# Kernel tuning notes

Hardware: AMD Instinct MI355X
Metric: run time of the kernel (lower is better)

Reference implementation:

```python
import jax, jax.numpy as jnp
import numpy as np

N_HEADS = 16
SEG_LEN = 512
MSG_LEN = 1536
T_TOTAL = SEG_LEN + MSG_LEN  # 2048


def _build_mask(T):
    # rows < SEG_LEN: attend to all cols < SEG_LEN (full, non-causal block)
    # rows >= SEG_LEN: standard causal (cols <= row)
    rows = jnp.arange(T)[:, None]
    cols = jnp.arange(T)[None, :]
    mask = jnp.where(rows < SEG_LEN, cols < SEG_LEN, cols <= rows)
    return mask  # [T, T] bool


def setup_inputs() -> dict:
    key = jax.random.key(0)
    k1, k2, k3 = jax.random.split(key, 3)
    B, T, E = 4, T_TOTAL, 1024
    x = jax.random.normal(k1, (B, T, E), dtype=jnp.float32)
    W_qkv = jax.random.normal(k2, (E, 3 * E), dtype=jnp.float32) * (1.0 / np.sqrt(E))
    b_qkv = jnp.zeros((3 * E,), dtype=jnp.float32)
    W_proj = jax.random.normal(k3, (E, E), dtype=jnp.float32) * (1.0 / np.sqrt(E))
    b_proj = jnp.zeros((E,), dtype=jnp.float32)
    return {"x": x, "W_qkv": W_qkv, "b_qkv": b_qkv, "W_proj": W_proj, "b_proj": b_proj}


def reference(x, W_qkv, b_qkv, W_proj, b_proj):
    B, T, E = x.shape
    H = N_HEADS
    D = E // H
    qkv = x @ W_qkv + b_qkv  # [B, T, 3E]
    q, k, v = jnp.split(qkv, 3, axis=-1)
    # [B, H, T, D]
    q = q.reshape(B, T, H, D).transpose(0, 2, 1, 3)
    k = k.reshape(B, T, H, D).transpose(0, 2, 1, 3)
    v = v.reshape(B, T, H, D).transpose(0, 2, 1, 3)
    att = jnp.einsum("bhqd,bhkd->bhqk", q, k) * (1.0 / np.sqrt(D))
    mask = _build_mask(T)  # [T, T]
    att = jnp.where(mask[None, None], att, jnp.float32(-jnp.inf))
    att = jax.nn.softmax(att, axis=-1)
    y = jnp.einsum("bhqk,bhkd->bhqd", att, v)
    y = y.transpose(0, 2, 1, 3).reshape(B, T, E)
    return y @ W_proj + b_proj
```

## Files before the change

### kernel.cpp

```cpp
#include <hip/hip_runtime.h>


typedef _Float16 f16;
typedef _Float16 f16x4 __attribute__((ext_vector_type(4)));
typedef _Float16 f16x8 __attribute__((ext_vector_type(8)));
typedef float f32x4 __attribute__((ext_vector_type(4)));

#define MFMA16x32(a, b, c) __builtin_amdgcn_mfma_f32_16x16x32_f16(a, b, c, 0, 0, 0)
#define MFMA16x16(a, b, c) __builtin_amdgcn_mfma_f32_16x16x16f16(a, b, c, 0, 0, 0)

__device__ __forceinline__ void gload_lds16(const void* g, void* l) {
  __builtin_amdgcn_global_load_lds(
      (__attribute__((address_space(1))) void*)g,
      (__attribute__((address_space(3))) void*)l, 16, 0, 0);
}


__global__ __launch_bounds__(256) void k_prep(
    const float* __restrict__ x, f16* __restrict__ xh,
    const float* __restrict__ Wq, f16* __restrict__ Wqt,
    const float* __restrict__ Wp, f16* __restrict__ Wpt) {
  __shared__ float tile[32][33];
  const int bid = blockIdx.x;
  if (bid < 8192) {
    int i = bid * 256 + threadIdx.x;
    float4 v = ((const float4*)x)[i];
    f16x4 o = {(f16)v.x, (f16)v.y, (f16)v.z, (f16)v.w};
    ((f16x4*)xh)[i] = o;
    return;
  }
  const float* W;
  f16* Wt;
  int Ndim, bx, by;
  if (bid < 8192 + 3072) {
    int r = bid - 8192;
    W = Wq; Wt = Wqt; Ndim = 3072; bx = r % 96; by = r / 96;
  } else {
    int r = bid - 11264;
    W = Wp; Wt = Wpt; Ndim = 1024; bx = r % 32; by = r / 32;
  }
  const int tx = threadIdx.x & 31, ty = threadIdx.x >> 5;
  const int n = bx * 32 + tx;
  const int k0 = by * 32;
  for (int j = ty; j < 32; j += 8)
    tile[j][tx] = W[(size_t)(k0 + j) * Ndim + n];
  __syncthreads();
  const int k = k0 + tx;
  for (int j = ty; j < 32; j += 8)
    Wt[(size_t)(bx * 32 + j) * 1024 + k] = (f16)tile[tx][j];
}


__global__ __launch_bounds__(512) void k_gemm_qkv(
    const f16* __restrict__ A, const f16* __restrict__ Bt,
    const float* __restrict__ bias,
    f16* __restrict__ Qo, f16* __restrict__ Ko, f16* __restrict__ Vo) {
  constexpr int KD = 1024;
  __shared__ __align__(16) f16 smem[(128 + 256) * 64];
  f16* As = smem;
  f16* Bs = smem + 128 * 64;
  const int tid = threadIdx.x;
  const int wave = tid >> 6, lane = tid & 63;
  const int g = lane >> 4, l16 = lane & 15;
  const int m0 = blockIdx.y * 128, n0 = blockIdx.x * 256;
  const int wm = (wave >> 2) * 64, wn = (wave & 3) * 64;
  const int srow = wave * 8 + (lane >> 3);
  const int skc = ((lane & 7) ^ (lane >> 3)) * 8;

  f32x4 acc[4][4] = {};

  for (int k0 = 0; k0 < KD; k0 += 64) {
    __syncthreads();
    for (int it = 0; it < 2; ++it)
      gload_lds16(A + (size_t)(m0 + it * 64 + srow) * KD + k0 + skc,
                  As + (it * 64 + wave * 8) * 64);
    for (int it = 0; it < 4; ++it)
      gload_lds16(Bt + (size_t)(n0 + it * 64 + srow) * KD + k0 + skc,
                  Bs + (it * 64 + wave * 8) * 64);
    __syncthreads();
    for (int kk = 0; kk < 64; kk += 32) {
      const int ks = kk >> 3;
      f16x8 af[4], bf[4];
      for (int mi = 0; mi < 4; ++mi) {
        int R = wm + mi * 16 + l16, sw = R & 7;
        af[mi] = *(const f16x8*)(As + R * 64 + ((ks + g) ^ sw) * 8);
      }
      for (int ni = 0; ni < 4; ++ni) {
        int R = wn + ni * 16 + l16, sw = R & 7;
        bf[ni] = *(const f16x8*)(Bs + R * 64 + ((ks + g) ^ sw) * 8);
      }
      for (int mi = 0; mi < 4; ++mi)
        for (int ni = 0; ni < 4; ++ni)
          acc[mi][ni] = MFMA16x32(af[mi], bf[ni], acc[mi][ni]);
    }
  }

  const int nsub = n0 + wn;
  const int part = nsub >> 10;
  const int h    = (nsub >> 6) & 15;
  const int mg   = m0 + wm;
  const int b    = mg >> 11;
  const int tb   = mg & 2047;
  const size_t bh = (size_t)(b * 16 + h);

  float bv[4];
  for (int ni = 0; ni < 4; ++ni) bv[ni] = bias[nsub + ni * 16 + l16];

  __syncthreads();
  f16* Es = smem + (wave & 3) * 4096;
  const int rrow = lane >> 3, rj = lane & 7;

  for (int phase = 0; phase < 2; ++phase) {
    if ((wave >> 2) == phase) {
      for (int mi = 0; mi < 4; ++mi)
        for (int ni = 0; ni < 4; ++ni)
          for (int r = 0; r < 4; ++r) {
            f16 hv = (f16)(acc[mi][ni][r] + bv[ni]);
            int mrow = mi * 16 + g * 4 + r, ncol = ni * 16 + l16;
            if (part == 2)
              Es[ncol * 64 + (mrow ^ ((ncol & 7) << 3))] = hv;
            else
              Es[mrow * 64 + (ncol ^ ((mrow & 7) << 3))] = hv;
          }
      for (int p = 0; p < 8; ++p) {
        int row = p * 8 + rrow;
        f16x8 vv = *(const f16x8*)(Es + row * 64 + (rj ^ (row & 7)) * 8);
        int rcol = rj * 8;
        if (part == 0)
          *(f16x8*)(Qo + (bh * 2048 + tb + row) * 64 + rcol) = vv;
        else if (part == 1)
          *(f16x8*)(Ko + (bh * 2048 + tb + row) * 64 + rcol) = vv;
        else
          *(f16x8*)(Vo + (bh * 64 + row) * 2048 + tb + rcol) = vv;
      }
    }
    __syncthreads();
  }
}


__global__ __launch_bounds__(256, 4) void k_attn(
    const f16* __restrict__ Q, const f16* __restrict__ Kb,
    const f16* __restrict__ Vt, f16* __restrict__ Y) {
  __shared__ __align__(16) f16 Ks[2][64 * 64];
  __shared__ __align__(16) f16 Vs[2][64 * 64];
  __shared__ float rs[4 * 32];

  const int tid = threadIdx.x;
  const int wave = tid >> 6, lane = tid & 63;
  const int g = lane >> 4, l16 = lane & 15;
  const int bh = blockIdx.x;
  const int b = bh >> 4, h = bh & 15;
  const int qt = 15 - blockIdx.y;
  const int q0 = qt * 128;
  const int nt = (qt < 4) ? 8 : (qt + 1) * 2;
  const int srowrel = lane >> 3;
  const int sc = (lane & 7) ^ srowrel;

  const f32x4 sinit = {-8.65617025f, -8.65617025f, -8.65617025f, -8.65617025f};

  f16x8 aq[2][2];
  for (int mi = 0; mi < 2; ++mi) {
    const f16* qrow =
        Q + ((size_t)bh * 2048 + q0 + wave * 32 + mi * 16 + l16) * 64 + g * 8;
    aq[mi][0] = *(const f16x8*)(qrow);
    aq[mi][1] = *(const f16x8*)(qrow + 32);
    for (int kb = 0; kb < 2; ++kb)
      aq[mi][kb] = aq[mi][kb] * (f16)0.18033688f;
  }

  f32x4 o[2][4] = {};
  float rsum[2] = {};

  for (int it = 0; it < 2; ++it) {
    int row = it * 32 + wave * 8 + srowrel;
    gload_lds16(Kb + ((size_t)bh * 2048 + row) * 64 + sc * 8,
                &Ks[0][(it * 32 + wave * 8) * 64]);
    gload_lds16(Vt + ((size_t)bh * 64 + row) * 2048 + sc * 8,
                &Vs[0][(it * 32 + wave * 8) * 64]);
  }
  __syncthreads();

  int cur = 0;
  for (int i = 0; i < nt; ++i) {
    if (i + 1 < nt) {
      const int kn0 = (i + 1) << 6;
      for (int it = 0; it < 2; ++it) {
        int row = it * 32 + wave * 8 + srowrel;
        gload_lds16(Kb + ((size_t)bh * 2048 + kn0 + row) * 64 + sc * 8,
                    &Ks[cur ^ 1][(it * 32 + wave * 8) * 64]);
        gload_lds16(Vt + ((size_t)bh * 64 + row) * 2048 + kn0 + sc * 8,
                    &Vs[cur ^ 1][(it * 32 + wave * 8) * 64]);
      }
    }

    const int kt0 = i << 6;
    const f16* Kc = Ks[cur];
    const f16* Vc = Vs[cur];

    f32x4 t[2][4];
    __builtin_amdgcn_s_setprio(1);
    for (int nb = 0; nb < 4; ++nb) {
      int R = nb * 16 + l16, sw = R & 7;
      f16x8 bk0 = *(const f16x8*)(Kc + R * 64 + ((0 + g) ^ sw) * 8);
      f16x8 bk1 = *(const f16x8*)(Kc + R * 64 + ((4 + g) ^ sw) * 8);
      for (int mi = 0; mi < 2; ++mi) {
        f32x4 acc = MFMA16x32(bk0, aq[mi][0], sinit);
        t[mi][nb] = MFMA16x32(bk1, aq[mi][1], acc);
      }
    }
    __builtin_amdgcn_s_setprio(0);

    const bool masked = (q0 >= 512) && (kt0 >= q0);
    f16x4 ap[4][2];
    for (int mi = 0; mi < 2; ++mi) {
      const int mrow = q0 + wave * 32 + mi * 16 + l16;
      for (int nb = 0; nb < 4; ++nb)
        for (int r = 0; r < 4; ++r) {
          float pv = __builtin_amdgcn_exp2f(t[mi][nb][r]);
          if (masked && (kt0 + nb * 16 + g * 4 + r > mrow)) pv = 0.f;
          rsum[mi] += pv;
          ap[nb][mi][r] = (f16)pv;
        }
    }

    __builtin_amdgcn_s_setprio(1);
    for (int db = 0; db < 4; ++db)
      for (int nb = 0; nb < 4; ++nb) {
        int R = db * 16 + l16, sw = R & 7;
        int c = nb * 2 + (g >> 1);
        f16x4 bv = *(const f16x4*)(Vc + R * 64 + (c ^ sw) * 8 + (g & 1) * 4);
        for (int mi = 0; mi < 2; ++mi)
          o[mi][db] = MFMA16x16(ap[nb][mi], bv, o[mi][db]);
      }
    __builtin_amdgcn_s_setprio(0);

    __syncthreads();
    cur ^= 1;
  }

  for (int mi = 0; mi < 2; ++mi) {
    rsum[mi] += __shfl_xor(rsum[mi], 16, 64);
    rsum[mi] += __shfl_xor(rsum[mi], 32, 64);
  }

  if (g == 0)
    for (int mi = 0; mi < 2; ++mi) rs[wave * 32 + mi * 16 + l16] = rsum[mi];
  float rinv[2][4];
  for (int mi = 0; mi < 2; ++mi)
    for (int r = 0; r < 4; ++r)
      rinv[mi][r] = 1.0f / rs[wave * 32 + mi * 16 + g * 4 + r];

  const size_t ybase = (size_t)b * 2048 + q0 + wave * 32;
  for (int mi = 0; mi < 2; ++mi)
    for (int db = 0; db < 4; ++db)
      for (int r = 0; r < 4; ++r)
        Y[(ybase + mi * 16 + g * 4 + r) * 1024 + h * 64 + db * 16 + l16] =
            (f16)(o[mi][db][r] * rinv[mi][r]);
}


__global__ __launch_bounds__(256) void k_gemm_proj(
    const f16* __restrict__ A, const f16* __restrict__ Bt,
    const float* __restrict__ bias, float* __restrict__ out) {
  constexpr int KD = 1024;
  __shared__ __align__(16) f16 As[128 * 64];
  __shared__ __align__(16) f16 Bs[128 * 64];
  const int tid = threadIdx.x;
  const int wave = tid >> 6, lane = tid & 63;
  const int g = lane >> 4, l16 = lane & 15;
  const int m0 = blockIdx.y * 128, n0 = blockIdx.x * 128;
  const int wm = (wave >> 1) * 64, wn = (wave & 1) * 64;
  const int srow = wave * 8 + (lane >> 3);
  const int skc = ((lane & 7) ^ (lane >> 3)) * 8;

  f32x4 acc[4][4] = {};

  for (int k0 = 0; k0 < KD; k0 += 64) {
    __syncthreads();
    for (int it = 0; it < 4; ++it) {
      gload_lds16(A + (size_t)(m0 + it * 32 + srow) * KD + k0 + skc,
                  As + (it * 32 + wave * 8) * 64);
      gload_lds16(Bt + (size_t)(n0 + it * 32 + srow) * KD + k0 + skc,
                  Bs + (it * 32 + wave * 8) * 64);
    }
    __syncthreads();
    for (int kk = 0; kk < 64; kk += 32) {
      const int ks = kk >> 3;
      f16x8 af[4], bf[4];
      for (int mi = 0; mi < 4; ++mi) {
        int R = wm + mi * 16 + l16, sw = R & 7;
        af[mi] = *(const f16x8*)(As + R * 64 + ((ks + g) ^ sw) * 8);
      }
      for (int ni = 0; ni < 4; ++ni) {
        int R = wn + ni * 16 + l16, sw = R & 7;
        bf[ni] = *(const f16x8*)(Bs + R * 64 + ((ks + g) ^ sw) * 8);
      }
      for (int mi = 0; mi < 4; ++mi)
        for (int ni = 0; ni < 4; ++ni)
          acc[mi][ni] = MFMA16x32(af[mi], bf[ni], acc[mi][ni]);
    }
  }

  float bv[4];
  for (int ni = 0; ni < 4; ++ni) bv[ni] = bias[n0 + wn + ni * 16 + l16];

  for (int mi = 0; mi < 4; ++mi)
    for (int ni = 0; ni < 4; ++ni)
      for (int r = 0; r < 4; ++r) {
        int m = m0 + wm + mi * 16 + g * 4 + r;
        int n = n0 + wn + ni * 16 + l16;
        out[(size_t)m * 1024 + n] = acc[mi][ni][r] + bv[ni];
      }
}


extern "C" void kernel_launch(void* const* d_in, const int* in_sizes, int n_in,
                              void* d_out, int out_size, void* d_ws,
                              size_t ws_size, hipStream_t stream) {
  const float* x      = (const float*)d_in[0];
  const float* W_qkv  = (const float*)d_in[1];
  const float* b_qkv  = (const float*)d_in[2];
  const float* W_proj = (const float*)d_in[3];
  const float* b_proj = (const float*)d_in[4];
  float* out = (float*)d_out;

  char* ws = (char*)d_ws;
  f16* xh    = (f16*)ws;   ws += (size_t)8192 * 1024 * 2;
  f16* Wqt   = (f16*)ws;   ws += (size_t)3072 * 1024 * 2;
  f16* Wpt   = (f16*)ws;   ws += (size_t)1024 * 1024 * 2;
  f16* Qb    = (f16*)ws;   ws += (size_t)64 * 2048 * 64 * 2;
  f16* Kb    = (f16*)ws;   ws += (size_t)64 * 2048 * 64 * 2;
  f16* Vt    = (f16*)ws;   ws += (size_t)64 * 64 * 2048 * 2;
  f16* Y = xh;

  k_prep<<<12288, 256, 0, stream>>>(x, xh, W_qkv, Wqt, W_proj, Wpt);
  k_gemm_qkv<<<dim3(12, 64), 512, 0, stream>>>(xh, Wqt, b_qkv, Qb, Kb, Vt);
  k_attn<<<dim3(64, 16), 256, 0, stream>>>(Qb, Kb, Vt, Y);
  k_gemm_proj<<<dim3(8, 64), 256, 0, stream>>>(Y, Wpt, b_proj, out);
}
```

Measured before the change: 263.9 us.

## Triple-buffer QKV GEMM LDS loads with async prefetch and single-phase epilogue

The QKV GEMM main loop moves from a single LDS buffer with two syncthreads per k-step to a three-slot ring. Global-to-LDS loads run two steps ahead, are interleaved with the MFMA sub-steps and are gated by explicit vmcnt waits and raw barriers. MFMA blocks get raised wave priority, and the epilogue writes all eight waves' tiles to separate LDS regions at once instead of in two phases. The cost is triple the shared memory (about 144KB), which limits occupancy, and a dependence on manual waitcnt counting being correct.

```diff
diff --git a/kernel.cpp b/kernel.cpp
--- a/kernel.cpp
+++ b/kernel.cpp
@@ -51,14 +51,13 @@
 }
 
 
-__global__ __launch_bounds__(512) void k_gemm_qkv(
+__global__ __launch_bounds__(512, 2) void k_gemm_qkv(
     const f16* __restrict__ A, const f16* __restrict__ Bt,
     const float* __restrict__ bias,
     f16* __restrict__ Qo, f16* __restrict__ Ko, f16* __restrict__ Vo) {
   constexpr int KD = 1024;
-  __shared__ __align__(16) f16 smem[(128 + 256) * 64];
-  f16* As = smem;
-  f16* Bs = smem + 128 * 64;
+  constexpr int SLOT = (128 + 256) * 64;
+  __shared__ __align__(16) f16 smem[3 * SLOT];
   const int tid = threadIdx.x;
   const int wave = tid >> 6, lane = tid & 63;
   const int g = lane >> 4, l16 = lane & 15;
@@ -69,30 +68,69 @@
 
   f32x4 acc[4][4] = {};
 
-  for (int k0 = 0; k0 < KD; k0 += 64) {
-    __syncthreads();
+  for (int t = 0; t < 2; ++t) {
+    f16* Sa = smem + t * SLOT;
+    f16* Sb = Sa + 128 * 64;
     for (int it = 0; it < 2; ++it)
-      gload_lds16(A + (size_t)(m0 + it * 64 + srow) * KD + k0 + skc,
-                  As + (it * 64 + wave * 8) * 64);
+      gload_lds16(A + (size_t)(m0 + it * 64 + srow) * KD + t * 64 + skc,
+                  Sa + (it * 64 + wave * 8) * 64);
     for (int it = 0; it < 4; ++it)
-      gload_lds16(Bt + (size_t)(n0 + it * 64 + srow) * KD + k0 + skc,
-                  Bs + (it * 64 + wave * 8) * 64);
-    __syncthreads();
-    for (int kk = 0; kk < 64; kk += 32) {
-      const int ks = kk >> 3;
+      gload_lds16(Bt + (size_t)(n0 + it * 64 + srow) * KD + t * 64 + skc,
+                  Sb + (it * 64 + wave * 8) * 64);
+  }
+  asm volatile("s_waitcnt vmcnt(6)" ::: "memory");
+  __builtin_amdgcn_s_barrier();
+
+  for (int u = 0; u < 16; ++u) {
+    const int s = u % 3;
+    f16* Sa = smem + s * SLOT;
+    f16* Sb = Sa + 128 * 64;
+    const bool pf = (u + 2) < 16;
+    f16* Pa = smem + ((u + 2) % 3) * SLOT;
+    f16* Pb = Pa + 128 * 64;
+    const int kp = (u + 2) * 64;
+
+    for (int kk = 0; kk < 2; ++kk) {
+      if (pf) {
+        if (kk == 0) {
+          gload_lds16(A + (size_t)(m0 + srow) * KD + kp + skc,
+                      Pa + (wave * 8) * 64);
+          gload_lds16(A + (size_t)(m0 + 64 + srow) * KD + kp + skc,
+                      Pa + (64 + wave * 8) * 64);
+          gload_lds16(Bt + (size_t)(n0 + srow) * KD + kp + skc,
+                      Pb + (wave * 8) * 64);
+        } else {
+          gload_lds16(Bt + (size_t)(n0 + 64 + srow) * KD + kp + skc,
+                      Pb + (64 + wave * 8) * 64);
+          gload_lds16(Bt + (size_t)(n0 + 128 + srow) * KD + kp + skc,
+                      Pb + (128 + wave * 8) * 64);
+          gload_lds16(Bt + (size_t)(n0 + 192 + srow) * KD + kp + skc,
+                      Pb + (192 + wave * 8) * 64);
+        }
+      }
+
+      const int ks = kk * 4;
       f16x8 af[4], bf[4];
       for (int mi = 0; mi < 4; ++mi) {
         int R = wm + mi * 16 + l16, sw = R & 7;
-        af[mi] = *(const f16x8*)(As + R * 64 + ((ks + g) ^ sw) * 8);
+        af[mi] = *(const f16x8*)(Sa + R * 64 + ((ks + g) ^ sw) * 8);
       }
       for (int ni = 0; ni < 4; ++ni) {
         int R = wn + ni * 16 + l16, sw = R & 7;
-        bf[ni] = *(const f16x8*)(Bs + R * 64 + ((ks + g) ^ sw) * 8);
-      }
+        bf[ni] = *(const f16x8*)(Sb + R * 64 + ((ks + g) ^ sw) * 8);
+      }
+      __builtin_amdgcn_s_setprio(1);
       for (int mi = 0; mi < 4; ++mi)
         for (int ni = 0; ni < 4; ++ni)
           acc[mi][ni] = MFMA16x32(af[mi], bf[ni], acc[mi][ni]);
-    }
+      __builtin_amdgcn_s_setprio(0);
+    }
+
+    if (u < 14)
+      asm volatile("s_waitcnt vmcnt(6)" ::: "memory");
+    else
+      asm volatile("s_waitcnt vmcnt(0)" ::: "memory");
+    __builtin_amdgcn_s_barrier();
   }
 
   const int nsub = n0 + wn;
@@ -106,35 +144,30 @@
   float bv[4];
   for (int ni = 0; ni < 4; ++ni) bv[ni] = bias[nsub + ni * 16 + l16];
 
-  __syncthreads();
-  f16* Es = smem + (wave & 3) * 4096;
+  f16* Es = smem + wave * 4096;
+
+  for (int mi = 0; mi < 4; ++mi)
+    for (int ni = 0; ni < 4; ++ni)
+      for (int r = 0; r < 4; ++r) {
+        f16 hv = (f16)(acc[mi][ni][r] + bv[ni]);
+        int mrow = mi * 16 + g * 4 + r, ncol = ni * 16 + l16;
+        if (part == 2)
+          Es[ncol * 64 + (mrow ^ ((ncol & 7) << 3))] = hv;
+        else
+          Es[mrow * 64 + (ncol ^ ((mrow & 7) << 3))] = hv;
+      }
+
   const int rrow = lane >> 3, rj = lane & 7;
-
-  for (int phase = 0; phase < 2; ++phase) {
-    if ((wave >> 2) == phase) {
-      for (int mi = 0; mi < 4; ++mi)
-        for (int ni = 0; ni < 4; ++ni)
-          for (int r = 0; r < 4; ++r) {
-            f16 hv = (f16)(acc[mi][ni][r] + bv[ni]);
-            int mrow = mi * 16 + g * 4 + r, ncol = ni * 16 + l16;
-            if (part == 2)
-              Es[ncol * 64 + (mrow ^ ((ncol & 7) << 3))] = hv;
-            else
-              Es[mrow * 64 + (ncol ^ ((mrow & 7) << 3))] = hv;
-          }
-      for (int p = 0; p < 8; ++p) {
-        int row = p * 8 + rrow;
-        f16x8 vv = *(const f16x8*)(Es + row * 64 + (rj ^ (row & 7)) * 8);
-        int rcol = rj * 8;
-        if (part == 0)
-          *(f16x8*)(Qo + (bh * 2048 + tb + row) * 64 + rcol) = vv;
-        else if (part == 1)
-          *(f16x8*)(Ko + (bh * 2048 + tb + row) * 64 + rcol) = vv;
-        else
-          *(f16x8*)(Vo + (bh * 64 + row) * 2048 + tb + rcol) = vv;
-      }
-    }
-    __syncthreads();
+  for (int p = 0; p < 8; ++p) {
+    int row = p * 8 + rrow;
+    f16x8 vv = *(const f16x8*)(Es + row * 64 + (rj ^ (row & 7)) * 8);
+    int rcol = rj * 8;
+    if (part == 0)
+      *(f16x8*)(Qo + (bh * 2048 + tb + row) * 64 + rcol) = vv;
+    else if (part == 1)
+      *(f16x8*)(Ko + (bh * 2048 + tb + row) * 64 + rcol) = vv;
+    else
+      *(f16x8*)(Vo + (bh * 64 + row) * 2048 + tb + rcol) = vv;
   }
 }
 
```

Result: faster. 252.2 us (-4.4%).
